# Kernel tuning notes

Measured on AMD Instinct MI355X. Metric: run time of the kernel, lower is better.

Reference implementation:

```python
import jax, jax.numpy as jnp
import numpy as np

T, H, I, E, S = 1024, 1024, 512, 64, 2  # tokens, hidden, intermediate, routed experts, shared experts
G, TOPK_GROUP, K = 8, 4, 8              # n_group, topk_group, num_experts_per_tok


def setup_inputs() -> dict:
    key = jax.random.key(0)
    ks = jax.random.split(key, 6)
    scale = 0.02
    x = jax.random.normal(ks[0], (T, H), dtype=jnp.float32)
    gate_w = jax.random.normal(ks[1], (E, H), dtype=jnp.float32) * scale   # MoEGate.weight [E,H]
    w_gu = jax.random.normal(ks[2], (E, H, 2 * I), dtype=jnp.float32) * scale  # gate_up_proj.weight.T per expert
    w_d = jax.random.normal(ks[3], (E, I, H), dtype=jnp.float32) * scale       # down_proj.weight.T per expert
    s_gu = jax.random.normal(ks[4], (S, H, 2 * I), dtype=jnp.float32) * scale  # shared experts
    s_d = jax.random.normal(ks[5], (S, I, H), dtype=jnp.float32) * scale
    return {"x": x, "gate_w": gate_w, "w_gu": w_gu, "w_d": w_d, "s_gu": s_gu, "s_d": s_d}


def _moe_forward(x, gate_w, w_gu, w_d, s_gu, s_d):
    t, h = x.shape
    e = w_gu.shape[0]
    i = w_gu.shape[2] // 2
    group_size = e // G

    # ---- shared experts (always active), summed ----
    sh = jnp.einsum('th,shf->stf', x, s_gu)            # [S,T,2I]
    shared = jnp.einsum('stf,sfh->th', jax.nn.silu(sh[..., :i]) * sh[..., i:], s_d)

    # ---- grouped top-k gating ----
    logits = x @ gate_w.T                               # [T,E]
    group_logits = logits.reshape(t, G, group_size)
    gw, gi = jax.lax.top_k(group_logits, TOPK_GROUP)    # [T,G,topk_group]
    gw = gw.reshape(t, G * TOPK_GROUP)
    gi = gi.reshape(t, G * TOPK_GROUP)
    topk_w, ti = jax.lax.top_k(gw, K)                   # [T,K]
    sel_group = ti // TOPK_GROUP
    expert_in_group = jnp.take_along_axis(gi, ti, axis=1)
    topk_idx = sel_group * group_size + expert_in_group # [T,K]
    topk_w = topk_w / (topk_w.sum(axis=-1, keepdims=True) + 1e-20)  # norm_topk_prob

    # ---- combine weights: sparse [T,E] scatter of top-k weights ----
    combine = jnp.zeros((t, e), x.dtype).at[jnp.arange(t)[:, None], topk_idx].add(topk_w)

    # ---- routed experts: dense grouped GEMM, zero-weighted where unselected ----
    gu = jnp.einsum('th,ehf->etf', x, w_gu)             # [E,T,2I]
    hidden = jax.nn.silu(gu[..., :i]) * gu[..., i:]     # [E,T,I]
    y = jnp.einsum('eti,eih->eth', hidden, w_d)         # [E,T,H]
    routed = jnp.einsum('eth,te->th', y, combine)

    return shared + routed


def reference(x, gate_w, w_gu, w_d, s_gu, s_d):
    return _moe_forward(x, gate_w, w_gu, w_d, s_gu, s_d)
```

## Files before the change

### kernel.cpp

```cpp
#include <hip/hip_runtime.h>
#include <hip/hip_bf16.h>

#define T_ 1024
#define H_ 1024
#define I_ 512
#define E_ 64
#define S_ 2
#define NJOB 66
#define KSEL 8
#define GRP 8
#define GSIZE 8
#define TKG 4
#define ROWS_TOTAL (T_*KSEL + S_*T_)

typedef __attribute__((ext_vector_type(8))) __bf16 bf16x8;
typedef __attribute__((ext_vector_type(8))) unsigned short u16x8;
typedef __attribute__((ext_vector_type(4))) unsigned short u16x4;
typedef __attribute__((ext_vector_type(4))) float f32x4;

__device__ inline unsigned short f2bf(float f) {
    unsigned u = __float_as_uint(f);
    u += 0x7FFFu + ((u >> 16) & 1u);
    return (unsigned short)(u >> 16);
}

__device__ inline void async16(const void* g, void* l) {
    __builtin_amdgcn_global_load_lds(
        (const __attribute__((address_space(1))) unsigned int*)g,
        (__attribute__((address_space(3))) unsigned int*)(uintptr_t)l,
        16, 0, 0);
}

__global__ __launch_bounds__(256) void cvt_x_kernel(const float* __restrict__ x,
                                                    unsigned short* __restrict__ xb) {
    int i = (blockIdx.x * 256 + threadIdx.x) * 4;
    f32x4 v = *(const f32x4*)(x + i);
    u16x4 o;
    o[0] = f2bf(v[0]); o[1] = f2bf(v[1]); o[2] = f2bf(v[2]); o[3] = f2bf(v[3]);
    *(u16x4*)(xb + i) = o;
}

__global__ __launch_bounds__(256) void cvtT_kernel(const float* __restrict__ src,
                                                   unsigned short* __restrict__ dst,
                                                   int K, int N) {
    int b = blockIdx.z;
    int n0 = blockIdx.x * 64, k0 = blockIdx.y * 64;
    __shared__ unsigned short Lt[64 * 68];
    const float* S = src + ((size_t)b * K + k0) * N + n0;
    unsigned short* D = dst + ((size_t)b * N + n0) * K + k0;
    int t = threadIdx.x;
    int kr = t >> 4;
    int nc = (t & 15) * 4;
#pragma unroll
    for (int p = 0; p < 4; ++p) {
        f32x4 v = *(const f32x4*)(S + (size_t)(kr + p * 16) * N + nc);
#pragma unroll
        for (int j = 0; j < 4; ++j) Lt[(nc + j) * 68 + kr + p * 16] = f2bf(v[j]);
    }
    __syncthreads();
    int nr = t >> 2;
    int kc = (t & 3) * 8;
#pragma unroll
    for (int p = 0; p < 2; ++p) {
        u16x8 o;
#pragma unroll
        for (int j = 0; j < 8; ++j) o[j] = Lt[nr * 68 + kc + p * 32 + j];
        *(u16x8*)(D + (size_t)nr * K + kc + p * 32) = o;
    }
}

__global__ __launch_bounds__(256) void gate_kernel(const float* __restrict__ x,
                                                   const float* __restrict__ gate_w,
                                                   int* __restrict__ counts,
                                                   int* __restrict__ topk_idx,
                                                   float* __restrict__ topk_w) {
    __shared__ float Wt[64 * 65];
    __shared__ float Xs[4 * 65];
    __shared__ float lg[4 * 65];

    int tid = threadIdx.x;
    int t0 = blockIdx.x * 4;
    int e = tid & 63;
    int wq = tid >> 6;
    int er = tid >> 2;
    int kq = (tid & 3) * 16;
    int xk = tid & 63;

    float acc = 0.f;
    for (int kc = 0; kc < 16; ++kc) {
        const float* wp = gate_w + er * H_ + kc * 64 + kq;
        f32x4 w0 = *(const f32x4*)(wp);
        f32x4 w1 = *(const f32x4*)(wp + 4);
        f32x4 w2 = *(const f32x4*)(wp + 8);
        f32x4 w3 = *(const f32x4*)(wp + 12);
        float xv = x[(size_t)(t0 + wq) * H_ + kc * 64 + xk];
        __syncthreads();
#pragma unroll
        for (int i = 0; i < 4; ++i) {
            Wt[(kq + i) * 65 + er] = w0[i];
            Wt[(kq + 4 + i) * 65 + er] = w1[i];
            Wt[(kq + 8 + i) * 65 + er] = w2[i];
            Wt[(kq + 12 + i) * 65 + er] = w3[i];
        }
        Xs[wq * 65 + xk] = xv;
        __syncthreads();
#pragma unroll 8
        for (int k = 0; k < 64; ++k)
            acc += Wt[k * 65 + e] * Xs[wq * 65 + k];
    }
    lg[wq * 65 + e] = acc;
    __syncthreads();

    if (tid < 4) {
        int t = t0 + tid;
        const float* L = &lg[tid * 65];
        float cv[GRP * TKG];
        int   ce[GRP * TKG];
        for (int g = 0; g < GRP; ++g) {
            unsigned used = 0;
            for (int r = 0; r < TKG; ++r) {
                float best = -INFINITY; int bi = 0;
                for (int j = 0; j < GSIZE; ++j) {
                    if (used & (1u << j)) continue;
                    float v = L[g * GSIZE + j];
                    if (v > best) { best = v; bi = j; }
                }
                used |= 1u << bi;
                cv[g * TKG + r] = best;
                ce[g * TKG + r] = g * GSIZE + bi;
            }
        }
        float sv[KSEL]; int si[KSEL];
        unsigned used = 0;
        float sum = 0.0f;
        for (int r = 0; r < KSEL; ++r) {
            float best = -INFINITY; int bi = 0;
            for (int j = 0; j < GRP * TKG; ++j) {
                if (used & (1u << j)) continue;
                if (cv[j] > best) { best = cv[j]; bi = j; }
            }
            used |= 1u << bi;
            sv[r] = best; si[r] = ce[bi];
            sum += best;
        }
        float inv = 1.0f / (sum + 1e-20f);
        for (int r = 0; r < KSEL; ++r) {
            topk_idx[t * KSEL + r] = si[r];
            topk_w[t * KSEL + r] = sv[r] * inv;
            atomicAdd(&counts[si[r]], 1);
        }
    }
}

__global__ void prefix_kernel(int* __restrict__ counts, int* __restrict__ offsets,
                              int* __restrict__ cursor) {
    if (threadIdx.x == 0) {
        counts[E_] = T_;
        counts[E_ + 1] = T_;
        int acc = 0;
        for (int j = 0; j < NJOB; ++j) {
            offsets[j] = acc;
            cursor[j] = acc;
            acc += counts[j];
        }
        offsets[NJOB] = acc;
    }
}

__global__ __launch_bounds__(256) void place_kernel(const int* __restrict__ topk_idx,
                                                    const float* __restrict__ topk_w,
                                                    const int* __restrict__ offsets,
                                                    int* __restrict__ cursor,
                                                    int* __restrict__ row_token,
                                                    float* __restrict__ row_w) {
    int p = blockIdx.x * 256 + threadIdx.x;
    if (p < T_ * KSEL) {
        int t = p >> 3;
        int e = topk_idx[p];
        int slot = atomicAdd(&cursor[e], 1);
        row_token[slot] = t;
        row_w[slot] = topk_w[p];
    } else if (p < T_ * KSEL + S_ * T_) {
        int q = p - T_ * KSEL;
        int s = q >> 10;
        int t = q & (T_ - 1);
        int slot = offsets[E_ + s] + t;
        row_token[slot] = t;
        row_w[slot] = 1.0f;
    }
}

__global__ __launch_bounds__(256) void gateup_kernel(const unsigned short* __restrict__ xb,
                                                     const unsigned short* __restrict__ wgu_t,
                                                     const unsigned short* __restrict__ sgu_t,
                                                     const int* __restrict__ offsets,
                                                     const int* __restrict__ row_token,
                                                     unsigned short* __restrict__ hidden) {
    int job = blockIdx.x, mt = blockIdx.y, nt = blockIdx.z;
    int seg = offsets[job];
    int cnt = offsets[job + 1] - seg;
    int m0 = mt * 128;
    if (m0 >= cnt) return;
    const unsigned short* Wt = (job < E_) ? (wgu_t + (size_t)job * (2 * I_) * H_)
                                          : (sgu_t + (size_t)(job - E_) * (2 * I_) * H_);
    int n0 = nt * 64;

    __shared__ unsigned short As[128 * 64];
    __shared__ unsigned short Bg[64 * 64];
    __shared__ unsigned short Bu[64 * 64];

    int tid = threadIdx.x;
    int wv = tid >> 6, lane = tid & 63, lrow = lane & 15, lq = lane >> 4;

    const unsigned short* asrc[4];
#pragma unroll
    for (int i = 0; i < 4; ++i) {
        int d = i * 256 + tid;
        int row = d >> 3;
        int kc = (d & 7) ^ (row & 7);
        int r = m0 + row;
        int gi = seg + (r < cnt ? r : 0);
        asrc[i] = xb + (size_t)row_token[gi] * H_ + kc * 8;
    }
    const unsigned short* bgsrc[2];
    const unsigned short* busrc[2];
#pragma unroll
    for (int i = 0; i < 2; ++i) {
        int d = i * 256 + tid;
        int n = d >> 3;
        int kc = (d & 7) ^ (n & 7);
        bgsrc[i] = Wt + (size_t)(n0 + n) * H_ + kc * 8;
        busrc[i] = Wt + (size_t)(I_ + n0 + n) * H_ + kc * 8;
    }

    f32x4 accg[2][4], accu[2][4];
    f32x4 zero = {0.f, 0.f, 0.f, 0.f};
#pragma unroll
    for (int a = 0; a < 2; ++a)
#pragma unroll
        for (int c = 0; c < 4; ++c) { accg[a][c] = zero; accu[a][c] = zero; }

    for (int kt = 0; kt < H_ / 64; ++kt) {
        int ko = kt * 64;
#pragma unroll
        for (int i = 0; i < 4; ++i)
            async16(asrc[i] + ko, &As[(i * 256 + tid) * 8]);
#pragma unroll
        for (int i = 0; i < 2; ++i) {
            async16(bgsrc[i] + ko, &Bg[(i * 256 + tid) * 8]);
            async16(busrc[i] + ko, &Bu[(i * 256 + tid) * 8]);
        }
        __syncthreads();

#pragma unroll
        for (int kk = 0; kk < 2; ++kk) {
            bf16x8 a[2];
#pragma unroll
            for (int rb = 0; rb < 2; ++rb) {
                int R = wv * 32 + rb * 16 + lrow;
                a[rb] = *(const bf16x8*)&As[R * 64 + (((lq + kk * 4) ^ (R & 7)) * 8)];
            }
#pragma unroll
            for (int cb = 0; cb < 4; ++cb) {
                int n = cb * 16 + lrow;
                int koff = ((lq + kk * 4) ^ (n & 7)) * 8;
                bf16x8 bg = *(const bf16x8*)&Bg[n * 64 + koff];
                bf16x8 bu = *(const bf16x8*)&Bu[n * 64 + koff];
#pragma unroll
                for (int rb = 0; rb < 2; ++rb) {
                    accg[rb][cb] = __builtin_amdgcn_mfma_f32_16x16x32_bf16(a[rb], bg, accg[rb][cb], 0, 0, 0);
                    accu[rb][cb] = __builtin_amdgcn_mfma_f32_16x16x32_bf16(a[rb], bu, accu[rb][cb], 0, 0, 0);
                }
            }
        }
        __syncthreads();
    }

#pragma unroll
    for (int rb = 0; rb < 2; ++rb)
#pragma unroll
        for (int cb = 0; cb < 4; ++cb)
#pragma unroll
            for (int r = 0; r < 4; ++r) {
                int row = wv * 32 + rb * 16 + lq * 4 + r;
                if (m0 + row < cnt) {
                    float g = accg[rb][cb][r];
                    float u = accu[rb][cb][r];
                    float hh = g / (1.0f + __expf(-g)) * u;
                    hidden[(size_t)(seg + m0 + row) * I_ + n0 + cb * 16 + lrow] = f2bf(hh);
                }
            }
}

__global__ __launch_bounds__(256) void down_kernel(const unsigned short* __restrict__ hidden,
                                                   const unsigned short* __restrict__ wd_t,
                                                   const unsigned short* __restrict__ sd_t,
                                                   const int* __restrict__ offsets,
                                                   const int* __restrict__ row_token,
                                                   const float* __restrict__ row_w,
                                                   float* __restrict__ out) {
    int job = blockIdx.x, mt = blockIdx.y, nt = blockIdx.z;
    int seg = offsets[job];
    int cnt = offsets[job + 1] - seg;
    int m0 = mt * 128;
    if (m0 >= cnt) return;
    const unsigned short* Wt = (job < E_) ? (wd_t + (size_t)job * H_ * I_)
                                          : (sd_t + (size_t)(job - E_) * H_ * I_);
    int n0 = nt * 64;

    __shared__ unsigned short As[128 * 64];
    __shared__ unsigned short Bs[64 * 64];

    int tid = threadIdx.x;
    int wv = tid >> 6, lane = tid & 63, lrow = lane & 15, lq = lane >> 4;

    const unsigned short* asrc[4];
#pragma unroll
    for (int i = 0; i < 4; ++i) {
        int d = i * 256 + tid;
        int row = d >> 3;
        int kc = (d & 7) ^ (row & 7);
        int r = m0 + row;
        int gi = seg + (r < cnt ? r : 0);
        asrc[i] = hidden + (size_t)gi * I_ + kc * 8;
    }
    const unsigned short* bsrc[2];
#pragma unroll
    for (int i = 0; i < 2; ++i) {
        int d = i * 256 + tid;
        int n = d >> 3;
        int kc = (d & 7) ^ (n & 7);
        bsrc[i] = Wt + (size_t)(n0 + n) * I_ + kc * 8;
    }

    f32x4 acc[2][4];
    f32x4 zero = {0.f, 0.f, 0.f, 0.f};
#pragma unroll
    for (int a = 0; a < 2; ++a)
#pragma unroll
        for (int c = 0; c < 4; ++c) acc[a][c] = zero;

    for (int kt = 0; kt < I_ / 64; ++kt) {
        int ko = kt * 64;
#pragma unroll
        for (int i = 0; i < 4; ++i)
            async16(asrc[i] + ko, &As[(i * 256 + tid) * 8]);
#pragma unroll
        for (int i = 0; i < 2; ++i)
            async16(bsrc[i] + ko, &Bs[(i * 256 + tid) * 8]);
        __syncthreads();

#pragma unroll
        for (int kk = 0; kk < 2; ++kk) {
            bf16x8 a[2];
#pragma unroll
            for (int rb = 0; rb < 2; ++rb) {
                int R = wv * 32 + rb * 16 + lrow;
                a[rb] = *(const bf16x8*)&As[R * 64 + (((lq + kk * 4) ^ (R & 7)) * 8)];
            }
#pragma unroll
            for (int cb = 0; cb < 4; ++cb) {
                int n = cb * 16 + lrow;
                bf16x8 b = *(const bf16x8*)&Bs[n * 64 + (((lq + kk * 4) ^ (n & 7)) * 8)];
#pragma unroll
                for (int rb = 0; rb < 2; ++rb)
                    acc[rb][cb] = __builtin_amdgcn_mfma_f32_16x16x32_bf16(a[rb], b, acc[rb][cb], 0, 0, 0);
            }
        }
        __syncthreads();
    }

#pragma unroll
    for (int rb = 0; rb < 2; ++rb)
#pragma unroll
        for (int r = 0; r < 4; ++r) {
            int row = wv * 32 + rb * 16 + lq * 4 + r;
            if (m0 + row < cnt) {
                int gi = seg + m0 + row;
                int tok = row_token[gi];
                float w = row_w[gi];
#pragma unroll
                for (int cb = 0; cb < 4; ++cb)
                    atomicAdd(&out[(size_t)tok * H_ + n0 + cb * 16 + lrow],
                              acc[rb][cb][r] * w);
            }
        }
}

extern "C" void kernel_launch(void* const* d_in, const int* in_sizes, int n_in,
                              void* d_out, int out_size, void* d_ws, size_t ws_size,
                              hipStream_t stream) {
    const float* x      = (const float*)d_in[0];
    const float* gate_w = (const float*)d_in[1];
    const float* w_gu   = (const float*)d_in[2];
    const float* w_d    = (const float*)d_in[3];
    const float* s_gu   = (const float*)d_in[4];
    const float* s_d    = (const float*)d_in[5];
    float* out = (float*)d_out;

    char* ws = (char*)d_ws;
    size_t off = 0;
    auto carve = [&](size_t bytes) -> void* {
        void* p = ws + off;
        off += (bytes + 255) & ~(size_t)255;
        return p;
    };
    int* counts            = (int*)carve(NJOB * 4);
    int* offsets           = (int*)carve((NJOB + 1) * 4);
    int* cursor            = (int*)carve(NJOB * 4);
    int* topk_idx          = (int*)carve(T_ * KSEL * 4);
    float* topk_w          = (float*)carve(T_ * KSEL * 4);
    int* row_token         = (int*)carve(ROWS_TOTAL * 4);
    float* row_w           = (float*)carve(ROWS_TOTAL * 4);
    unsigned short* xb     = (unsigned short*)carve((size_t)T_ * H_ * 2);
    unsigned short* hidden = (unsigned short*)carve((size_t)ROWS_TOTAL * I_ * 2);
    unsigned short* wgu_t  = (unsigned short*)carve((size_t)E_ * (2 * I_) * H_ * 2);
    unsigned short* wd_t   = (unsigned short*)carve((size_t)E_ * H_ * I_ * 2);
    unsigned short* sgu_t  = (unsigned short*)carve((size_t)S_ * (2 * I_) * H_ * 2);
    unsigned short* sd_t   = (unsigned short*)carve((size_t)S_ * H_ * I_ * 2);

    hipMemsetAsync(out, 0, (size_t)T_ * H_ * 4, stream);
    hipMemsetAsync(counts, 0, NJOB * 4, stream);

    cvt_x_kernel<<<(T_ * H_ / 4) / 256, 256, 0, stream>>>(x, xb);
    cvtT_kernel<<<dim3((2 * I_) / 64, H_ / 64, E_), 256, 0, stream>>>(w_gu, wgu_t, H_, 2 * I_);
    cvtT_kernel<<<dim3(H_ / 64, I_ / 64, E_), 256, 0, stream>>>(w_d, wd_t, I_, H_);
    cvtT_kernel<<<dim3((2 * I_) / 64, H_ / 64, S_), 256, 0, stream>>>(s_gu, sgu_t, H_, 2 * I_);
    cvtT_kernel<<<dim3(H_ / 64, I_ / 64, S_), 256, 0, stream>>>(s_d, sd_t, I_, H_);

    gate_kernel<<<T_ / 4, 256, 0, stream>>>(x, gate_w, counts, topk_idx, topk_w);
    prefix_kernel<<<1, 64, 0, stream>>>(counts, offsets, cursor);
    place_kernel<<<(ROWS_TOTAL + 255) / 256, 256, 0, stream>>>(topk_idx, topk_w, offsets,
                                                               cursor, row_token, row_w);
    gateup_kernel<<<dim3(NJOB, T_ / 128, I_ / 64), 256, 0, stream>>>(xb, wgu_t, sgu_t, offsets,
                                                                     row_token, hidden);
    down_kernel<<<dim3(NJOB, T_ / 128, H_ / 64), 256, 0, stream>>>(hidden, wd_t, sd_t, offsets,
                                                                   row_token, row_w, out);
}
```

Before: 692.0 us.

## Fuse fp32 weight transpose and bf16 conversion into grouped GEMM B-tile loads

Drops the separate cvtT passes that converted and transposed every expert weight to bf16 in workspace before the GEMMs. The gate-up and down kernels now read fp32 weights directly, convert them to bf16 in registers, and write them transposed and swizzled into LDS. The next k-tile is prefetched into registers during the current iteration. This removes a full extra read and write of all expert weights per call, but weights are re-read and re-converted by every M-tile block, and fp32 loads double the B-side global traffic.

```diff
diff --git a/kernel.cpp b/kernel.cpp
--- a/kernel.cpp
+++ b/kernel.cpp
@@ -24,6 +24,12 @@
     return (unsigned short)(u >> 16);
 }
 
+__device__ inline unsigned pk2bf(float a, float b) {
+    unsigned short ua = __builtin_bit_cast(unsigned short, (__bf16)a);
+    unsigned short ub = __builtin_bit_cast(unsigned short, (__bf16)b);
+    return (unsigned)ua | ((unsigned)ub << 16);
+}
+
 __device__ inline void async16(const void* g, void* l) {
     __builtin_amdgcn_global_load_lds(
         (const __attribute__((address_space(1))) unsigned int*)g,
@@ -38,35 +44,6 @@
     u16x4 o;
     o[0] = f2bf(v[0]); o[1] = f2bf(v[1]); o[2] = f2bf(v[2]); o[3] = f2bf(v[3]);
     *(u16x4*)(xb + i) = o;
-}
-
-__global__ __launch_bounds__(256) void cvtT_kernel(const float* __restrict__ src,
-                                                   unsigned short* __restrict__ dst,
-                                                   int K, int N) {
-    int b = blockIdx.z;
-    int n0 = blockIdx.x * 64, k0 = blockIdx.y * 64;
-    __shared__ unsigned short Lt[64 * 68];
-    const float* S = src + ((size_t)b * K + k0) * N + n0;
-    unsigned short* D = dst + ((size_t)b * N + n0) * K + k0;
-    int t = threadIdx.x;
-    int kr = t >> 4;
-    int nc = (t & 15) * 4;
-#pragma unroll
-    for (int p = 0; p < 4; ++p) {
-        f32x4 v = *(const f32x4*)(S + (size_t)(kr + p * 16) * N + nc);
-#pragma unroll
-        for (int j = 0; j < 4; ++j) Lt[(nc + j) * 68 + kr + p * 16] = f2bf(v[j]);
-    }
-    __syncthreads();
-    int nr = t >> 2;
-    int kc = (t & 3) * 8;
-#pragma unroll
-    for (int p = 0; p < 2; ++p) {
-        u16x8 o;
-#pragma unroll
-        for (int j = 0; j < 8; ++j) o[j] = Lt[nr * 68 + kc + p * 32 + j];
-        *(u16x8*)(D + (size_t)nr * K + kc + p * 32) = o;
-    }
 }
 
 __global__ __launch_bounds__(256) void gate_kernel(const float* __restrict__ x,
@@ -191,8 +168,8 @@
 }
 
 __global__ __launch_bounds__(256) void gateup_kernel(const unsigned short* __restrict__ xb,
-                                                     const unsigned short* __restrict__ wgu_t,
-                                                     const unsigned short* __restrict__ sgu_t,
+                                                     const float* __restrict__ w_gu,
+                                                     const float* __restrict__ s_gu,
                                                      const int* __restrict__ offsets,
                                                      const int* __restrict__ row_token,
                                                      unsigned short* __restrict__ hidden) {
@@ -201,8 +178,8 @@
     int cnt = offsets[job + 1] - seg;
     int m0 = mt * 128;
     if (m0 >= cnt) return;
-    const unsigned short* Wt = (job < E_) ? (wgu_t + (size_t)job * (2 * I_) * H_)
-                                          : (sgu_t + (size_t)(job - E_) * (2 * I_) * H_);
+    const float* W = (job < E_) ? (w_gu + (size_t)job * H_ * (2 * I_))
+                                : (s_gu + (size_t)(job - E_) * H_ * (2 * I_));
     int n0 = nt * 64;
 
     __shared__ unsigned short As[128 * 64];
@@ -222,16 +199,12 @@
         int gi = seg + (r < cnt ? r : 0);
         asrc[i] = xb + (size_t)row_token[gi] * H_ + kc * 8;
     }
-    const unsigned short* bgsrc[2];
-    const unsigned short* busrc[2];
-#pragma unroll
-    for (int i = 0; i < 2; ++i) {
-        int d = i * 256 + tid;
-        int n = d >> 3;
-        int kc = (d & 7) ^ (n & 7);
-        bgsrc[i] = Wt + (size_t)(n0 + n) * H_ + kc * 8;
-        busrc[i] = Wt + (size_t)(I_ + n0 + n) * H_ + kc * 8;
-    }
+
+    int bk = (tid & 15) * 4;
+    int bn = (tid >> 4) * 4;
+    int c0 = bk >> 3;
+    int h8 = (bk & 4) * 2;
+    const float* bbase = W + (size_t)bk * (2 * I_) + n0 + bn;
 
     f32x4 accg[2][4], accu[2][4];
     f32x4 zero = {0.f, 0.f, 0.f, 0.f};
@@ -240,15 +213,38 @@
 #pragma unroll
         for (int c = 0; c < 4; ++c) { accg[a][c] = zero; accu[a][c] = zero; }
 
+    f32x4 g[4], u[4];
+#pragma unroll
+    for (int r = 0; r < 4; ++r) {
+        g[r] = *(const f32x4*)(bbase + (size_t)r * (2 * I_));
+        u[r] = *(const f32x4*)(bbase + (size_t)r * (2 * I_) + I_);
+    }
+
     for (int kt = 0; kt < H_ / 64; ++kt) {
         int ko = kt * 64;
 #pragma unroll
         for (int i = 0; i < 4; ++i)
             async16(asrc[i] + ko, &As[(i * 256 + tid) * 8]);
-#pragma unroll
-        for (int i = 0; i < 2; ++i) {
-            async16(bgsrc[i] + ko, &Bg[(i * 256 + tid) * 8]);
-            async16(busrc[i] + ko, &Bu[(i * 256 + tid) * 8]);
+
+#pragma unroll
+        for (int j = 0; j < 4; ++j) {
+            int nj = bn + j;
+            int byteoff = nj * 128 + ((c0 ^ (nj & 7)) * 16) + h8;
+            uint2 vg, vu;
+            vg.x = pk2bf(g[0][j], g[1][j]); vg.y = pk2bf(g[2][j], g[3][j]);
+            vu.x = pk2bf(u[0][j], u[1][j]); vu.y = pk2bf(u[2][j], u[3][j]);
+            *(uint2*)((char*)Bg + byteoff) = vg;
+            *(uint2*)((char*)Bu + byteoff) = vu;
+        }
+
+        {
+            int kn = ((kt + 1) & 15) * 64;
+            const float* bp = bbase + (size_t)kn * (2 * I_);
+#pragma unroll
+            for (int r = 0; r < 4; ++r) {
+                g[r] = *(const f32x4*)(bp + (size_t)r * (2 * I_));
+                u[r] = *(const f32x4*)(bp + (size_t)r * (2 * I_) + I_);
+            }
         }
         __syncthreads();
 
@@ -284,17 +280,17 @@
             for (int r = 0; r < 4; ++r) {
                 int row = wv * 32 + rb * 16 + lq * 4 + r;
                 if (m0 + row < cnt) {
-                    float g = accg[rb][cb][r];
-                    float u = accu[rb][cb][r];
-                    float hh = g / (1.0f + __expf(-g)) * u;
+                    float gg = accg[rb][cb][r];
+                    float uu = accu[rb][cb][r];
+                    float hh = gg / (1.0f + __expf(-gg)) * uu;
                     hidden[(size_t)(seg + m0 + row) * I_ + n0 + cb * 16 + lrow] = f2bf(hh);
                 }
             }
 }
 
 __global__ __launch_bounds__(256) void down_kernel(const unsigned short* __restrict__ hidden,
-                                                   const unsigned short* __restrict__ wd_t,
-                                                   const unsigned short* __restrict__ sd_t,
+                                                   const float* __restrict__ w_d,
+                                                   const float* __restrict__ s_d,
                                                    const int* __restrict__ offsets,
                                                    const int* __restrict__ row_token,
                                                    const float* __restrict__ row_w,
@@ -304,8 +300,8 @@
     int cnt = offsets[job + 1] - seg;
     int m0 = mt * 128;
     if (m0 >= cnt) return;
-    const unsigned short* Wt = (job < E_) ? (wd_t + (size_t)job * H_ * I_)
-                                          : (sd_t + (size_t)(job - E_) * H_ * I_);
+    const float* W = (job < E_) ? (w_d + (size_t)job * I_ * H_)
+                                : (s_d + (size_t)(job - E_) * I_ * H_);
     int n0 = nt * 64;
 
     __shared__ unsigned short As[128 * 64];
@@ -324,14 +320,12 @@
         int gi = seg + (r < cnt ? r : 0);
         asrc[i] = hidden + (size_t)gi * I_ + kc * 8;
     }
-    const unsigned short* bsrc[2];
-#pragma unroll
-    for (int i = 0; i < 2; ++i) {
-        int d = i * 256 + tid;
-        int n = d >> 3;
-        int kc = (d & 7) ^ (n & 7);
-        bsrc[i] = Wt + (size_t)(n0 + n) * I_ + kc * 8;
-    }
+
+    int bk = (tid & 15) * 4;
+    int bn = (tid >> 4) * 4;
+    int c0 = bk >> 3;
+    int h8 = (bk & 4) * 2;
+    const float* bbase = W + (size_t)bk * H_ + n0 + bn;
 
     f32x4 acc[2][4];
     f32x4 zero = {0.f, 0.f, 0.f, 0.f};
@@ -340,14 +334,32 @@
 #pragma unroll
         for (int c = 0; c < 4; ++c) acc[a][c] = zero;
 
+    f32x4 d4[4];
+#pragma unroll
+    for (int r = 0; r < 4; ++r)
+        d4[r] = *(const f32x4*)(bbase + (size_t)r * H_);
+
     for (int kt = 0; kt < I_ / 64; ++kt) {
         int ko = kt * 64;
 #pragma unroll
         for (int i = 0; i < 4; ++i)
             async16(asrc[i] + ko, &As[(i * 256 + tid) * 8]);
-#pragma unroll
-        for (int i = 0; i < 2; ++i)
-            async16(bsrc[i] + ko, &Bs[(i * 256 + tid) * 8]);
+
+#pragma unroll
+        for (int j = 0; j < 4; ++j) {
+            int nj = bn + j;
+            int byteoff = nj * 128 + ((c0 ^ (nj & 7)) * 16) + h8;
+            uint2 vb;
+            vb.x = pk2bf(d4[0][j], d4[1][j]); vb.y = pk2bf(d4[2][j], d4[3][j]);
+            *(uint2*)((char*)Bs + byteoff) = vb;
+        }
+        {
+            int kn = ((kt + 1) & 7) * 64;
+            const float* bp = bbase + (size_t)kn * H_;
+#pragma unroll
+            for (int r = 0; r < 4; ++r)
+                d4[r] = *(const f32x4*)(bp + (size_t)r * H_);
+        }
         __syncthreads();
 
 #pragma unroll
@@ -414,26 +426,17 @@
     float* row_w           = (float*)carve(ROWS_TOTAL * 4);
     unsigned short* xb     = (unsigned short*)carve((size_t)T_ * H_ * 2);
     unsigned short* hidden = (unsigned short*)carve((size_t)ROWS_TOTAL * I_ * 2);
-    unsigned short* wgu_t  = (unsigned short*)carve((size_t)E_ * (2 * I_) * H_ * 2);
-    unsigned short* wd_t   = (unsigned short*)carve((size_t)E_ * H_ * I_ * 2);
-    unsigned short* sgu_t  = (unsigned short*)carve((size_t)S_ * (2 * I_) * H_ * 2);
-    unsigned short* sd_t   = (unsigned short*)carve((size_t)S_ * H_ * I_ * 2);
 
     hipMemsetAsync(out, 0, (size_t)T_ * H_ * 4, stream);
     hipMemsetAsync(counts, 0, NJOB * 4, stream);
 
     cvt_x_kernel<<<(T_ * H_ / 4) / 256, 256, 0, stream>>>(x, xb);
-    cvtT_kernel<<<dim3((2 * I_) / 64, H_ / 64, E_), 256, 0, stream>>>(w_gu, wgu_t, H_, 2 * I_);
-    cvtT_kernel<<<dim3(H_ / 64, I_ / 64, E_), 256, 0, stream>>>(w_d, wd_t, I_, H_);
-    cvtT_kernel<<<dim3((2 * I_) / 64, H_ / 64, S_), 256, 0, stream>>>(s_gu, sgu_t, H_, 2 * I_);
-    cvtT_kernel<<<dim3(H_ / 64, I_ / 64, S_), 256, 0, stream>>>(s_d, sd_t, I_, H_);
-
     gate_kernel<<<T_ / 4, 256, 0, stream>>>(x, gate_w, counts, topk_idx, topk_w);
     prefix_kernel<<<1, 64, 0, stream>>>(counts, offsets, cursor);
     place_kernel<<<(ROWS_TOTAL + 255) / 256, 256, 0, stream>>>(topk_idx, topk_w, offsets,
                                                                cursor, row_token, row_w);
-    gateup_kernel<<<dim3(NJOB, T_ / 128, I_ / 64), 256, 0, stream>>>(xb, wgu_t, sgu_t, offsets,
+    gateup_kernel<<<dim3(NJOB, T_ / 128, I_ / 64), 256, 0, stream>>>(xb, w_gu, s_gu, offsets,
                                                                      row_token, hidden);
-    down_kernel<<<dim3(NJOB, T_ / 128, H_ / 64), 256, 0, stream>>>(hidden, wd_t, sd_t, offsets,
+    down_kernel<<<dim3(NJOB, T_ / 128, H_ / 64), 256, 0, stream>>>(hidden, w_d, s_d, offsets,
                                                                    row_token, row_w, out);
 }
```

Result: faster. 626.3 us (-9.5%).
